# Optimization experiments

Measured on AMD Instinct MI355X. Metric: run time of the kernel, lower is better.

Reference implementation:

```python
import jax, jax.numpy as jnp
import numpy as np

EPS = 1e-12  # matches torch F.normalize eps


def _l2norm(v, axis):
    return v / jnp.maximum(jnp.linalg.norm(v, axis=axis, keepdims=True), EPS)


def setup_inputs() -> dict:
    key = jax.random.key(0)
    k1, k2, k3 = jax.random.split(key, 3)
    B, C, H, W, K = 32, 512, 40, 40, 64
    x = jax.random.normal(k1, (B, C, H, W), dtype=jnp.float32)
    centroids = jax.random.uniform(k2, (K, C), dtype=jnp.float32)  # torch.rand init
    assign_w = jax.random.normal(k3, (K, C), dtype=jnp.float32)    # 1x1 conv weight, no bias
    return {"x": x, "centroids": centroids, "assign_w": assign_w}


def reference(x, centroids, assign_w):
    # x: [B, C, H, W]; centroids/assign_w: [K, C]
    B, C, H, W = x.shape
    x = _l2norm(x, axis=1)                      # channel-wise L2 normalize
    xf = x.reshape(B, C, H * W)                 # [B, C, N]
    # 1x1 conv == per-pixel matmul with [K, C] weight
    logits = jnp.einsum('kc,bcn->bkn', assign_w, xf)
    a = jax.nn.softmax(logits, axis=1)          # softmax over clusters, [B, K, N]
    # vlad[b,k,c] = sum_n a[b,k,n] * (x[b,c,n] - centroid[k,c])
    #            = (a @ x^T)[b,k,c] - centroid[k,c] * sum_n a[b,k,n]
    vlad = jnp.einsum('bkn,bcn->bkc', a, xf) - a.sum(axis=-1)[..., None] * centroids[None]
    vlad = _l2norm(vlad, axis=2)                # intra-normalization per cluster
    vlad = vlad.reshape(B, -1)                  # [B, K*C]
    return _l2norm(vlad, axis=1)                # global L2 normalize
```

## Files before the change

kernel.cpp:

```cpp
#include <hip/hip_runtime.h>
#include <hip/hip_bf16.h>
#include <math.h>

#define BB   32
#define CC   512
#define NPIX 1600
#define KK   64
#define NT   25
#define EPSF 1e-12f

typedef __attribute__((ext_vector_type(8))) short bf16x8;
typedef __attribute__((ext_vector_type(4))) float f32x4;
#define MFMA16 __builtin_amdgcn_mfma_f32_16x16x32_bf16

__device__ __forceinline__ ushort f2bf(float f) {
    __hip_bfloat16 h = __float2bfloat16(f);
    return *reinterpret_cast<ushort*>(&h);
}
__device__ __forceinline__ uint pk2bf(float a, float b) {
    return (uint)f2bf(a) | ((uint)f2bf(b) << 16);
}

__global__ __launch_bounds__(256) void k_wprep(const float* __restrict__ w,
                                               ushort* __restrict__ wb) {
    int i = blockIdx.x * 256 + threadIdx.x;
    float2 v = *(const float2*)&w[(size_t)i * 2];
    ((uint*)wb)[i] = pk2bf(v.x, v.y);
}

__global__ __launch_bounds__(256) void k_gemm1m(const float* __restrict__ x,
                                                const ushort* __restrict__ wb,
                                                ushort* __restrict__ a_t,
                                                float* __restrict__ asum_p) {
    int tile = blockIdx.x, b = blockIdx.y;
    int n0 = tile * 64;
    __shared__ __align__(16) ushort Xs[2][64 * 32];
    __shared__ __align__(16) ushort Wsh[2][64 * 32];
    __shared__ __align__(16) float red[16 * 64];
    __shared__ __align__(16) float asw[4 * 64];
    __shared__ __align__(16) float ivs[64];
    int t = threadIdx.x;
    int lane = t & 63, wv = t >> 6;
    int nlo = lane & 15, khi = lane >> 4;
    int sc2 = (t & 15) * 2;
    int sn4 = (t >> 4) * 4;
    int wk  = t >> 2;
    int wc8 = (t & 3) * 8;
    const float* xb = x + (size_t)b * CC * NPIX + n0;
    f32x4 acc[4] = {};
    float ss[4] = {0.f, 0.f, 0.f, 0.f};

    float4 xa, xc; uint4 wp;
    xa = *(const float4*)&xb[(size_t)sc2 * NPIX + sn4];
    xc = *(const float4*)&xb[(size_t)(sc2 + 1) * NPIX + sn4];
    wp = *(const uint4*)&wb[(size_t)wk * CC + wc8];
    {
        uint* XU = (uint*)Xs[0]; uint* WU = (uint*)Wsh[0];
        float va[4] = {xa.x, xa.y, xa.z, xa.w};
        float vc[4] = {xc.x, xc.y, xc.z, xc.w};
#pragma unroll
        for (int j = 0; j < 4; ++j) {
            ss[j] += va[j] * va[j] + vc[j] * vc[j];
            int row = sn4 + j;
            int gp = ((t & 15) >> 2) ^ ((row >> 1) & 3);
            XU[row * 16 + gp * 4 + (t & 3)] = pk2bf(va[j], vc[j]);
        }
        int gp = (t & 3) ^ ((wk >> 1) & 3);
        *(uint4*)&WU[wk * 16 + gp * 4] = wp;
    }
    __syncthreads();

    int cur = 0;
    for (int it = 0; it < 16; ++it) {
        bool pre = (it < 15);
        if (pre) {
            int c0 = (it + 1) * 32;
            xa = *(const float4*)&xb[(size_t)(c0 + sc2) * NPIX + sn4];
            xc = *(const float4*)&xb[(size_t)(c0 + sc2 + 1) * NPIX + sn4];
            wp = *(const uint4*)&wb[(size_t)wk * CC + c0 + wc8];
        }
        {
            const ushort* Xc = Xs[cur];
            const ushort* Wc = Wsh[cur];
            int rn = wv * 16 + nlo;
            int gB = khi ^ ((rn >> 1) & 3);
            bf16x8 bfr = *(const bf16x8*)&Xc[rn * 32 + gB * 8];
#pragma unroll
            for (int kf = 0; kf < 4; ++kf) {
                int rk = kf * 16 + nlo;
                int gA = khi ^ ((rk >> 1) & 3);
                bf16x8 afr = *(const bf16x8*)&Wc[rk * 32 + gA * 8];
                acc[kf] = MFMA16(afr, bfr, acc[kf], 0, 0, 0);
            }
        }
        if (pre) {
            uint* XU = (uint*)Xs[cur ^ 1]; uint* WU = (uint*)Wsh[cur ^ 1];
            float va[4] = {xa.x, xa.y, xa.z, xa.w};
            float vc[4] = {xc.x, xc.y, xc.z, xc.w};
#pragma unroll
            for (int j = 0; j < 4; ++j) {
                ss[j] += va[j] * va[j] + vc[j] * vc[j];
                int row = sn4 + j;
                int gp = ((t & 15) >> 2) ^ ((row >> 1) & 3);
                XU[row * 16 + gp * 4 + (t & 3)] = pk2bf(va[j], vc[j]);
            }
            int gp = (t & 3) ^ ((wk >> 1) & 3);
            *(uint4*)&WU[wk * 16 + gp * 4] = wp;
        }
        __syncthreads();
        cur ^= 1;
    }

#pragma unroll
    for (int j = 0; j < 4; ++j) red[(t & 15) * 64 + sn4 + j] = ss[j];
    __syncthreads();
    if (t < 64) {
        float s = 0.f;
#pragma unroll
        for (int i = 0; i < 16; ++i) s += red[i * 64 + t];
        ivs[t] = 1.f / fmaxf(sqrtf(s), EPSF);
    }
    __syncthreads();

    int nloc = wv * 16 + nlo;
    float invl = ivs[nloc];

    float lv[4][4];
    float mm = -1e30f;
#pragma unroll
    for (int kf = 0; kf < 4; ++kf)
#pragma unroll
        for (int r = 0; r < 4; ++r) {
            lv[kf][r] = acc[kf][r] * invl;
            mm = fmaxf(mm, lv[kf][r]);
        }
    mm = fmaxf(mm, __shfl_xor(mm, 16));
    mm = fmaxf(mm, __shfl_xor(mm, 32));
    float ev[4][4], s = 0.f;
#pragma unroll
    for (int kf = 0; kf < 4; ++kf)
#pragma unroll
        for (int r = 0; r < 4; ++r) {
            ev[kf][r] = expf(lv[kf][r] - mm);
            s += ev[kf][r];
        }
    s += __shfl_xor(s, 16);
    s += __shfl_xor(s, 32);
    float sd = 1.f / s;

    float av[4][4];
#pragma unroll
    for (int kf = 0; kf < 4; ++kf)
#pragma unroll
        for (int r = 0; r < 4; ++r) av[kf][r] = ev[kf][r] * sd;
#pragma unroll
    for (int off = 1; off < 16; off <<= 1)
#pragma unroll
        for (int kf = 0; kf < 4; ++kf)
#pragma unroll
            for (int r = 0; r < 4; ++r) av[kf][r] += __shfl_xor(av[kf][r], off);
    if (nlo == 0) {
#pragma unroll
        for (int kf = 0; kf < 4; ++kf)
#pragma unroll
            for (int r = 0; r < 4; ++r)
                asw[wv * 64 + kf * 16 + khi * 4 + r] = av[kf][r];
    }

    ushort* ab = a_t + (size_t)b * KK * NPIX;
#pragma unroll
    for (int kf = 0; kf < 4; ++kf)
#pragma unroll
        for (int r = 0; r < 4; ++r) {
            int k = kf * 16 + khi * 4 + r;
            ab[(size_t)k * NPIX + n0 + nloc] = f2bf(ev[kf][r] * sd * invl);
        }
    __syncthreads();
    if (t < 64) {
        float a4 = asw[t] + asw[64 + t] + asw[128 + t] + asw[192 + t];
        asum_p[((size_t)b * KK + t) * NT + tile] = a4;
    }
}

__global__ __launch_bounds__(256) void k_vladm(const ushort* __restrict__ a_t,
                                               const float* __restrict__ x,
                                               float* __restrict__ part,
                                               int nchunk) {
    int c0 = blockIdx.x * 64;
    int s  = blockIdx.y;
    int b  = blockIdx.z;
    __shared__ __align__(16) ushort Ash[2][64 * 32];
    __shared__ __align__(16) ushort Xsh[2][64 * 32];
    int t = threadIdx.x;
    int lane = t & 63, wv = t >> 6;
    int sk  = t >> 2;
    int sn8 = (t & 3) * 8;
    const ushort* ab = a_t + (size_t)b * KK * NPIX;
    const float*  xb = x + (size_t)b * CC * NPIX;
    f32x4 acc[4] = {};
    int nbase = s * nchunk;
    int niters = nchunk / 32;

    uint4 ar; float4 x0, x1;
    ar = *(const uint4*)&ab[(size_t)sk * NPIX + nbase + sn8];
    x0 = *(const float4*)&xb[(size_t)(c0 + sk) * NPIX + nbase + sn8];
    x1 = *(const float4*)&xb[(size_t)(c0 + sk) * NPIX + nbase + sn8 + 4];
    {
        uint* AU = (uint*)Ash[0]; uint* XU = (uint*)Xsh[0];
        int gp = (t & 3) ^ ((sk >> 1) & 3);
        *(uint4*)&AU[sk * 16 + gp * 4] = ar;
        uint4 xp;
        xp.x = pk2bf(x0.x, x0.y); xp.y = pk2bf(x0.z, x0.w);
        xp.z = pk2bf(x1.x, x1.y); xp.w = pk2bf(x1.z, x1.w);
        *(uint4*)&XU[sk * 16 + gp * 4] = xp;
    }
    __syncthreads();

    int cur = 0;
    for (int it = 0; it < niters; ++it) {
        bool pre = (it + 1 < niters);
        if (pre) {
            int ng = nbase + (it + 1) * 32;
            ar = *(const uint4*)&ab[(size_t)sk * NPIX + ng + sn8];
            x0 = *(const float4*)&xb[(size_t)(c0 + sk) * NPIX + ng + sn8];
            x1 = *(const float4*)&xb[(size_t)(c0 + sk) * NPIX + ng + sn8 + 4];
        }
        {
            const ushort* Ac = Ash[cur];
            const ushort* Xc = Xsh[cur];
            int rc = wv * 16 + (lane & 15);
            int gB = (lane >> 4) ^ ((rc >> 1) & 3);
            bf16x8 bfr = *(const bf16x8*)&Xc[rc * 32 + gB * 8];
#pragma unroll
            for (int kf = 0; kf < 4; ++kf) {
                int rk = kf * 16 + (lane & 15);
                int gA = (lane >> 4) ^ ((rk >> 1) & 3);
                bf16x8 afr = *(const bf16x8*)&Ac[rk * 32 + gA * 8];
                acc[kf] = MFMA16(afr, bfr, acc[kf], 0, 0, 0);
            }
        }
        if (pre) {
            uint* AU = (uint*)Ash[cur ^ 1]; uint* XU = (uint*)Xsh[cur ^ 1];
            int gp = (t & 3) ^ ((sk >> 1) & 3);
            *(uint4*)&AU[sk * 16 + gp * 4] = ar;
            uint4 xp;
            xp.x = pk2bf(x0.x, x0.y); xp.y = pk2bf(x0.z, x0.w);
            xp.z = pk2bf(x1.x, x1.y); xp.w = pk2bf(x1.z, x1.w);
            *(uint4*)&XU[sk * 16 + gp * 4] = xp;
        }
        __syncthreads();
        cur ^= 1;
    }

#pragma unroll
    for (int kf = 0; kf < 4; ++kf)
#pragma unroll
        for (int r = 0; r < 4; ++r) {
            int k = kf * 16 + (lane >> 4) * 4 + r;
            int c = c0 + wv * 16 + (lane & 15);
            part[(((size_t)s * BB + b) * KK + k) * CC + c] = acc[kf][r];
        }
}

__global__ __launch_bounds__(256) void k_asum(const float* __restrict__ asum_p,
                                              float* __restrict__ asum) {
    int row = blockIdx.x * 256 + threadIdx.x;
    const float* p = asum_p + (size_t)row * NT;
    float s = 0.f;
#pragma unroll
    for (int i = 0; i < NT; ++i) s += p[i];
    asum[row] = s;
}

__global__ __launch_bounds__(256) void k_intra(const float* __restrict__ part, int ns,
                                               const float* __restrict__ asum,
                                               const float* __restrict__ cent,
                                               float* __restrict__ out,
                                               float* __restrict__ bsum) {
    int row = blockIdx.x;
    int b = row >> 6, k = row & 63;
    int t = threadIdx.x;
    float v0 = 0.f, v1 = 0.f;
    for (int s2 = 0; s2 < ns; ++s2) {
        const float* p = part + (((size_t)s2 * BB + b) * KK + k) * CC;
        v0 += p[t];
        v1 += p[t + 256];
    }
    float as = asum[row];
    v0 -= as * cent[k * CC + t];
    v1 -= as * cent[k * CC + t + 256];
    float ssq = v0 * v0 + v1 * v1;
#pragma unroll
    for (int off = 32; off; off >>= 1) ssq += __shfl_down(ssq, off, 64);
    __shared__ float red[4];
    __shared__ float s_inv;
    if ((t & 63) == 0) red[t >> 6] = ssq;
    __syncthreads();
    if (t == 0) {
        float sm = red[0] + red[1] + red[2] + red[3];
        float inv = 1.f / fmaxf(sqrtf(sm), EPSF);
        s_inv = inv;
        atomicAdd(&bsum[b], sm * inv * inv);
    }
    __syncthreads();
    float inv = s_inv;
    out[(size_t)row * CC + t]       = v0 * inv;
    out[(size_t)row * CC + t + 256] = v1 * inv;
}

__global__ __launch_bounds__(256) void k_scale(float* __restrict__ out,
                                               const float* __restrict__ bsum) {
    int idx = blockIdx.x * 256 + threadIdx.x;
    int b = idx >> 15;
    out[idx] *= 1.f / fmaxf(sqrtf(bsum[b]), EPSF);
}

extern "C" void kernel_launch(void* const* d_in, const int* in_sizes, int n_in,
                              void* d_out, int out_size, void* d_ws, size_t ws_size,
                              hipStream_t stream) {
    const float* x    = (const float*)d_in[0];
    const float* cent = (const float*)d_in[1];
    const float* w    = (const float*)d_in[2];
    float* out = (float*)d_out;

    char* wsb = (char*)d_ws;
    const size_t oa_at   = 0;
    const size_t oa_wb   = oa_at + (size_t)BB * KK * NPIX * 2;
    const size_t oa_ap   = oa_wb + (size_t)KK * CC * 2;
    const size_t oa_as   = oa_ap + (size_t)BB * KK * NT * 4;
    const size_t oa_bsum = oa_as + (size_t)BB * KK * 4;
    const size_t oa_part = oa_bsum + 128;
    ushort* a_t   = (ushort*)(wsb + oa_at);
    ushort* wb    = (ushort*)(wsb + oa_wb);
    float* asum_p = (float*)(wsb + oa_ap);
    float* asum   = (float*)(wsb + oa_as);
    float* bsum   = (float*)(wsb + oa_bsum);

    const size_t pbytes = (size_t)BB * KK * CC * 4;
    int ns = 0;
    const int cand[3] = {5, 2, 1};
    for (int i = 0; i < 3; ++i) {
        if (oa_part + (size_t)cand[i] * pbytes <= ws_size) { ns = cand[i]; break; }
    }
    float* part = (ns > 0) ? (float*)(wsb + oa_part) : out;
    if (ns == 0) ns = 1;
    int nchunk = NPIX / ns;

    hipMemsetAsync(bsum, 0, BB * sizeof(float), stream);

    k_wprep <<<dim3((KK * CC / 2) / 256), 256, 0, stream>>>(w, wb);
    k_gemm1m<<<dim3(NT, BB), 256, 0, stream>>>(x, wb, a_t, asum_p);
    k_vladm <<<dim3(CC / 64, ns, BB), 256, 0, stream>>>(a_t, x, part, nchunk);
    k_asum  <<<dim3(BB * KK / 256), 256, 0, stream>>>(asum_p, asum);
    k_intra <<<dim3(BB * KK), 256, 0, stream>>>(part, ns, asum, cent, out, bsum);
    k_scale <<<dim3((BB * KK * CC) / 256), 256, 0, stream>>>(out, bsum);
}
```

Before: 93.47 us.

## Fuse weight conversion and asum reduction into consumers, deepen gemm1 prefetch

Drops the separate weight-to-bf16 prep kernel; k_gemm1m now loads fp32 weights and converts them while staging into shared memory. It also removes the k_asum kernel by having k_intra sum the per-tile partial assignment sums itself. The gemm1 main loop is fully unrolled and prefetches global data two iterations ahead in a register double buffer. This saves two kernel launches and their dependency gaps, at the cost of redundant weight conversion in every block and more register pressure.

```diff
diff --git a/kernel.cpp b/kernel.cpp
--- a/kernel.cpp
+++ b/kernel.cpp
@@ -21,15 +21,8 @@
     return (uint)f2bf(a) | ((uint)f2bf(b) << 16);
 }
 
-__global__ __launch_bounds__(256) void k_wprep(const float* __restrict__ w,
-                                               ushort* __restrict__ wb) {
-    int i = blockIdx.x * 256 + threadIdx.x;
-    float2 v = *(const float2*)&w[(size_t)i * 2];
-    ((uint*)wb)[i] = pk2bf(v.x, v.y);
-}
-
 __global__ __launch_bounds__(256) void k_gemm1m(const float* __restrict__ x,
-                                                const ushort* __restrict__ wb,
+                                                const float* __restrict__ w,
                                                 ushort* __restrict__ a_t,
                                                 float* __restrict__ asum_p) {
     int tile = blockIdx.x, b = blockIdx.y;
@@ -50,38 +43,49 @@
     f32x4 acc[4] = {};
     float ss[4] = {0.f, 0.f, 0.f, 0.f};
 
-    float4 xa, xc; uint4 wp;
-    xa = *(const float4*)&xb[(size_t)sc2 * NPIX + sn4];
-    xc = *(const float4*)&xb[(size_t)(sc2 + 1) * NPIX + sn4];
-    wp = *(const uint4*)&wb[(size_t)wk * CC + wc8];
-    {
-        uint* XU = (uint*)Xs[0]; uint* WU = (uint*)Wsh[0];
-        float va[4] = {xa.x, xa.y, xa.z, xa.w};
-        float vc[4] = {xc.x, xc.y, xc.z, xc.w};
-#pragma unroll
-        for (int j = 0; j < 4; ++j) {
-            ss[j] += va[j] * va[j] + vc[j] * vc[j];
-            int row = sn4 + j;
-            int gp = ((t & 15) >> 2) ^ ((row >> 1) & 3);
-            XU[row * 16 + gp * 4 + (t & 3)] = pk2bf(va[j], vc[j]);
-        }
-        int gp = (t & 3) ^ ((wk >> 1) & 3);
-        *(uint4*)&WU[wk * 16 + gp * 4] = wp;
-    }
-    __syncthreads();
-
-    int cur = 0;
+    float4 xa[2], xc[2], wa[2], wc2[2];
+
+#define LOADQ(it_, sl_)                                                      \
+    {                                                                        \
+        int cb_ = (it_) * 32;                                                \
+        xa[sl_]  = *(const float4*)&xb[(size_t)(cb_ + sc2) * NPIX + sn4];    \
+        xc[sl_]  = *(const float4*)&xb[(size_t)(cb_ + sc2 + 1) * NPIX + sn4];\
+        wa[sl_]  = *(const float4*)&w[(size_t)wk * CC + cb_ + wc8];          \
+        wc2[sl_] = *(const float4*)&w[(size_t)wk * CC + cb_ + wc8 + 4];      \
+    }
+#define STOREQ(it_, sl_)                                                     \
+    {                                                                        \
+        uint* XU = (uint*)Xs[(it_) & 1];                                     \
+        uint* WU = (uint*)Wsh[(it_) & 1];                                    \
+        float va_[4] = {xa[sl_].x, xa[sl_].y, xa[sl_].z, xa[sl_].w};         \
+        float vc_[4] = {xc[sl_].x, xc[sl_].y, xc[sl_].z, xc[sl_].w};         \
+        _Pragma("unroll")                                                    \
+        for (int j = 0; j < 4; ++j) {                                        \
+            ss[j] += va_[j] * va_[j] + vc_[j] * vc_[j];                      \
+            int row_ = sn4 + j;                                              \
+            int gp_ = ((t & 15) >> 2) ^ ((row_ >> 1) & 3);                   \
+            XU[row_ * 16 + gp_ * 4 + (t & 3)] = pk2bf(va_[j], vc_[j]);       \
+        }                                                                    \
+        uint4 wp_;                                                           \
+        wp_.x = pk2bf(wa[sl_].x,  wa[sl_].y);                                \
+        wp_.y = pk2bf(wa[sl_].z,  wa[sl_].w);                                \
+        wp_.z = pk2bf(wc2[sl_].x, wc2[sl_].y);                               \
+        wp_.w = pk2bf(wc2[sl_].z, wc2[sl_].w);                               \
+        int gw_ = (t & 3) ^ ((wk >> 1) & 3);                                 \
+        *(uint4*)&WU[wk * 16 + gw_ * 4] = wp_;                               \
+    }
+
+    LOADQ(0, 0);
+    LOADQ(1, 1);
+    STOREQ(0, 0);
+    __syncthreads();
+
+#pragma unroll
     for (int it = 0; it < 16; ++it) {
-        bool pre = (it < 15);
-        if (pre) {
-            int c0 = (it + 1) * 32;
-            xa = *(const float4*)&xb[(size_t)(c0 + sc2) * NPIX + sn4];
-            xc = *(const float4*)&xb[(size_t)(c0 + sc2 + 1) * NPIX + sn4];
-            wp = *(const uint4*)&wb[(size_t)wk * CC + c0 + wc8];
-        }
+        if (it + 2 < 16) LOADQ(it + 2, it & 1);
         {
-            const ushort* Xc = Xs[cur];
-            const ushort* Wc = Wsh[cur];
+            const ushort* Xc = Xs[it & 1];
+            const ushort* Wc = Wsh[it & 1];
             int rn = wv * 16 + nlo;
             int gB = khi ^ ((rn >> 1) & 3);
             bf16x8 bfr = *(const bf16x8*)&Xc[rn * 32 + gB * 8];
@@ -93,23 +97,11 @@
                 acc[kf] = MFMA16(afr, bfr, acc[kf], 0, 0, 0);
             }
         }
-        if (pre) {
-            uint* XU = (uint*)Xs[cur ^ 1]; uint* WU = (uint*)Wsh[cur ^ 1];
-            float va[4] = {xa.x, xa.y, xa.z, xa.w};
-            float vc[4] = {xc.x, xc.y, xc.z, xc.w};
-#pragma unroll
-            for (int j = 0; j < 4; ++j) {
-                ss[j] += va[j] * va[j] + vc[j] * vc[j];
-                int row = sn4 + j;
-                int gp = ((t & 15) >> 2) ^ ((row >> 1) & 3);
-                XU[row * 16 + gp * 4 + (t & 3)] = pk2bf(va[j], vc[j]);
-            }
-            int gp = (t & 3) ^ ((wk >> 1) & 3);
-            *(uint4*)&WU[wk * 16 + gp * 4] = wp;
-        }
+        if (it + 1 < 16) STOREQ(it + 1, (it + 1) & 1);
         __syncthreads();
-        cur ^= 1;
-    }
+    }
+#undef LOADQ
+#undef STOREQ
 
 #pragma unroll
     for (int j = 0; j < 4; ++j) red[(t & 15) * 64 + sn4 + j] = ss[j];
@@ -262,18 +254,8 @@
         }
 }
 
-__global__ __launch_bounds__(256) void k_asum(const float* __restrict__ asum_p,
-                                              float* __restrict__ asum) {
-    int row = blockIdx.x * 256 + threadIdx.x;
-    const float* p = asum_p + (size_t)row * NT;
-    float s = 0.f;
-#pragma unroll
-    for (int i = 0; i < NT; ++i) s += p[i];
-    asum[row] = s;
-}
-
 __global__ __launch_bounds__(256) void k_intra(const float* __restrict__ part, int ns,
-                                               const float* __restrict__ asum,
+                                               const float* __restrict__ asum_p,
                                                const float* __restrict__ cent,
                                                float* __restrict__ out,
                                                float* __restrict__ bsum) {
@@ -286,7 +268,9 @@
         v0 += p[t];
         v1 += p[t + 256];
     }
-    float as = asum[row];
+    float as = 0.f;
+#pragma unroll
+    for (int i = 0; i < NT; ++i) as += asum_p[(size_t)row * NT + i];
     v0 -= as * cent[k * CC + t];
     v1 -= as * cent[k * CC + t + 256];
     float ssq = v0 * v0 + v1 * v1;
@@ -325,15 +309,11 @@
 
     char* wsb = (char*)d_ws;
     const size_t oa_at   = 0;
-    const size_t oa_wb   = oa_at + (size_t)BB * KK * NPIX * 2;
-    const size_t oa_ap   = oa_wb + (size_t)KK * CC * 2;
-    const size_t oa_as   = oa_ap + (size_t)BB * KK * NT * 4;
-    const size_t oa_bsum = oa_as + (size_t)BB * KK * 4;
+    const size_t oa_ap   = oa_at + (size_t)BB * KK * NPIX * 2;
+    const size_t oa_bsum = oa_ap + (size_t)BB * KK * NT * 4;
     const size_t oa_part = oa_bsum + 128;
     ushort* a_t   = (ushort*)(wsb + oa_at);
-    ushort* wb    = (ushort*)(wsb + oa_wb);
     float* asum_p = (float*)(wsb + oa_ap);
-    float* asum   = (float*)(wsb + oa_as);
     float* bsum   = (float*)(wsb + oa_bsum);
 
     const size_t pbytes = (size_t)BB * KK * CC * 4;
@@ -348,10 +328,8 @@
 
     hipMemsetAsync(bsum, 0, BB * sizeof(float), stream);
 
-    k_wprep <<<dim3((KK * CC / 2) / 256), 256, 0, stream>>>(w, wb);
-    k_gemm1m<<<dim3(NT, BB), 256, 0, stream>>>(x, wb, a_t, asum_p);
+    k_gemm1m<<<dim3(NT, BB), 256, 0, stream>>>(x, w, a_t, asum_p);
     k_vladm <<<dim3(CC / 64, ns, BB), 256, 0, stream>>>(a_t, x, part, nchunk);
-    k_asum  <<<dim3(BB * KK / 256), 256, 0, stream>>>(asum_p, asum);
-    k_intra <<<dim3(BB * KK), 256, 0, stream>>>(part, ns, asum, cent, out, bsum);
+    k_intra <<<dim3(BB * KK), 256, 0, stream>>>(part, ns, asum_p, cent, out, bsum);
     k_scale <<<dim3((BB * KK * CC) / 256), 256, 0, stream>>>(out, bsum);
 }
```

Result: faster. 89.30 us (-4.5%).
